# Kernel optimization log

Hardware: AMD Instinct MI355X
Metric: run time of the kernel (lower is better)

## Reference

```python
import jax, jax.numpy as jnp
import numpy as np

D_MODEL = 768
D_HEAD = 64
BATCH = 2
SEQ = 4096


def setup_inputs() -> dict:
    key = jax.random.key(0)
    k1, k2, k3, k4, k5 = jax.random.split(key, 5)
    x = jax.random.normal(k1, (BATCH, SEQ, D_MODEL), dtype=jnp.float32)
    # causal mask as the module expects: (seq_len, seq_len) float, 1 where attend allowed
    mask = jnp.tril(jnp.ones((SEQ, SEQ), dtype=jnp.float32))
    # weights initialized like the module: randn / sqrt(d_model)
    scale = 1.0 / np.sqrt(D_MODEL)
    Wq = jax.random.normal(k2, (D_HEAD, D_MODEL), dtype=jnp.float32) * scale
    Wk = jax.random.normal(k3, (D_HEAD, D_MODEL), dtype=jnp.float32) * scale
    Wv = jax.random.normal(k4, (D_HEAD, D_MODEL), dtype=jnp.float32) * scale
    Wo = jax.random.normal(k5, (D_MODEL, D_HEAD), dtype=jnp.float32) * scale
    return {"x": x, "mask": mask, "Wq": Wq, "Wk": Wk, "Wv": Wv, "Wo": Wo}


def reference(x, mask, Wq, Wk, Wv, Wo):
    # q,k,v: (B, S, d_head); Linear with weight (out,in) => x @ W.T
    q = jnp.einsum('bsm,hm->bsh', x, Wq)
    k = jnp.einsum('bsm,hm->bsh', x, Wk)
    v = jnp.einsum('bsm,hm->bsh', x, Wv)
    scores = jnp.einsum('bqd,bkd->bqk', q, k) / np.sqrt(D_HEAD)  # (B,S,S)
    seq_len = x.shape[1]
    m = mask[:seq_len, :seq_len]
    # faithful to the torch code: tril(scores) - 1e10 * (1 - mask)
    scores = jnp.tril(scores) - 1e10 * (1.0 - m)
    attn = jax.nn.softmax(scores, axis=-1)
    z = jnp.einsum('bqk,bkd->bqd', attn, v)  # (B,S,d_head)
    out = jnp.einsum('bsh,mh->bsm', z, Wo)   # (B,S,d_model)
    return out
```

## Files before the change

### kernel.cpp

```cpp
#include <hip/hip_runtime.h>
#include <stdint.h>

#define SEQ 4096
#define DM 768
#define DH 64

typedef __attribute__((ext_vector_type(8))) short short8;
typedef __attribute__((ext_vector_type(4))) short short4v;
typedef __attribute__((ext_vector_type(4))) float f32x4;
typedef __attribute__((ext_vector_type(2))) uint32_t uint2v;

#define LOG2E 1.4426950408889634f

static __device__ __forceinline__ short bf16r(float f) {
  union { float f; uint32_t u; } v; v.f = f;
  uint32_t u = v.u;
  return (short)((u + 0x7FFFu + ((u >> 16) & 1u)) >> 16);
}

static __device__ __forceinline__ float bf16f(uint16_t u) {
  union { uint32_t u; float f; } v; v.u = ((uint32_t)u) << 16;
  return v.f;
}

static __device__ __forceinline__ uint32_t cvtpk(float a, float b) {
  uint32_t r;
  asm("v_cvt_pk_bf16_f32 %0, %1, %2" : "=v"(r) : "v"(a), "v"(b));
  return r;
}

static __device__ __forceinline__ int swz(int row, int b) {
  return row * 128 + (b ^ ((row & 7) << 4));
}

static __device__ __forceinline__ void glds16(const void* g, void* l) {
  __builtin_amdgcn_global_load_lds(
      (const __attribute__((address_space(1))) uint32_t*)g,
      (__attribute__((address_space(3))) uint32_t*)l, 16, 0, 0);
}

__global__ __launch_bounds__(256) void convert_w(
    const float* __restrict__ Wq, const float* __restrict__ Wk,
    const float* __restrict__ Wv, const float* __restrict__ Wo,
    uint16_t* __restrict__ Wbp, uint16_t* __restrict__ Wob) {
  int id = blockIdx.x * 256 + threadIdx.x;
  if (id < 18432) {
    int nh = id / 9216, rem = id % 9216;
    int t = rem / 768, rem2 = rem % 768;
    int r = rem2 >> 3, g = rem2 & 7;
    int row = nh * 96 + r;
    const float* src = (row < 64) ? (Wq + (size_t)row * DM)
                     : (row < 128) ? (Wk + (size_t)(row - 64) * DM)
                                   : (Wv + (size_t)(row - 128) * DM);
    const float sc = (row < 64) ? (0.125f * LOG2E) : 1.0f;
    float4 v0 = *(const float4*)(src + t * 64 + g * 8);
    float4 v1 = *(const float4*)(src + t * 64 + g * 8 + 4);
    union { uint32_t u[4]; short8 s; } pk;
    pk.u[0] = cvtpk(v0.x * sc, v0.y * sc);
    pk.u[1] = cvtpk(v0.z * sc, v0.w * sc);
    pk.u[2] = cvtpk(v1.x * sc, v1.y * sc);
    pk.u[3] = cvtpk(v1.z * sc, v1.w * sc);
    char* dst = (char*)Wbp + (size_t)nh * 147456 + t * 12288 + swz(r, g * 16);
    *(short8*)dst = pk.s;
  } else if (id < 30720) {
    int tt = id - 18432;
    int row = tt >> 4, c4 = tt & 15;
    float4 v = *(const float4*)(Wo + (size_t)row * DH + c4 * 4);
    short4v pk = { bf16r(v.x), bf16r(v.y), bf16r(v.z), bf16r(v.w) };
    *(short4v*)(Wob + (size_t)row * DH + c4 * 4) = pk;
  }
}

__global__ __launch_bounds__(256) void qkv_proj(
    const float* __restrict__ x, const uint16_t* __restrict__ Wbp,
    uint16_t* __restrict__ qg, uint16_t* __restrict__ kg, uint16_t* __restrict__ vg) {
  __shared__ char smem[49152] __attribute__((aligned(16)));
  const int tid = threadIdx.x;
  const int lane = tid & 63, wv = tid >> 6;
  const int l15 = lane & 15, l4 = lane >> 4;
  const int row0 = blockIdx.x * 32;
  const int nh = blockIdx.y;
  const char* wsrc = (const char*)Wbp + (size_t)nh * 147456;

  const int xr = tid >> 4, xc4 = tid & 15;
  const int mh = wv & 1, ng = wv >> 1;

  const float* xp0 = x + (size_t)(row0 + xr) * DM + xc4 * 4;
  const float* xp1 = x + (size_t)(row0 + 16 + xr) * DM + xc4 * 4;

  f32x4 acc[3];
  #pragma unroll
  for (int j = 0; j < 3; ++j) acc[j] = (f32x4){0.f, 0.f, 0.f, 0.f};

  float4 xrg[2][2];
  xrg[0][0] = *(const float4*)(xp0);
  xrg[0][1] = *(const float4*)(xp1);
  #pragma unroll
  for (int i = 0; i < 3; ++i)
    glds16(wsrc + i * 1024 + wv * 3072 + lane * 16,
           smem + 12288 + wv * 3072 + i * 1024);
  __builtin_amdgcn_sched_barrier(0);
  xrg[1][0] = *(const float4*)(xp0 + 64);
  xrg[1][1] = *(const float4*)(xp1 + 64);
  #pragma unroll
  for (int i = 0; i < 3; ++i)
    glds16(wsrc + 12288 + wv * 3072 + i * 1024 + lane * 16,
           smem + 12288 + 12288 + wv * 3072 + i * 1024);
  __builtin_amdgcn_sched_barrier(0);
  {
    uint2v p0 = { cvtpk(xrg[0][0].x, xrg[0][0].y), cvtpk(xrg[0][0].z, xrg[0][0].w) };
    *(uint2v*)(smem + swz(xr, xc4 * 8)) = p0;
    uint2v p1 = { cvtpk(xrg[0][1].x, xrg[0][1].y), cvtpk(xrg[0][1].z, xrg[0][1].w) };
    *(uint2v*)(smem + swz(xr + 16, xc4 * 8)) = p1;
  }

  #pragma unroll
  for (int t = 0; t < 12; ++t) {
    asm volatile("s_waitcnt lgkmcnt(0)" ::: "memory");
    if (t < 11) {
      asm volatile("s_waitcnt vmcnt(5)" ::: "memory");
    } else {
      asm volatile("s_waitcnt vmcnt(0)" ::: "memory");
    }
    __builtin_amdgcn_s_barrier();
    if (t < 10) {
      const int k2 = (t + 2) * 64;
      xrg[t & 1][0] = *(const float4*)(xp0 + k2);
      xrg[t & 1][1] = *(const float4*)(xp1 + k2);
      #pragma unroll
      for (int i = 0; i < 3; ++i)
        glds16(wsrc + (t + 2) * 12288 + wv * 3072 + i * 1024 + lane * 16,
               smem + 12288 + ((t + 2) % 3) * 12288 + wv * 3072 + i * 1024);
      __builtin_amdgcn_sched_barrier(0);
    }
    {
      char* Xl = smem + (t % 3) * 4096;
      char* Wl = smem + 12288 + (t % 3) * 12288;
      #pragma unroll
      for (int kc = 0; kc < 2; ++kc) {
        short8 af = *(const short8*)(Xl + swz(mh * 16 + l15, kc * 64 + l4 * 16));
        #pragma unroll
        for (int j = 0; j < 3; ++j) {
          int tl = ng * 3 + j;
          short8 bfv = *(const short8*)(Wl + swz(tl * 16 + l15, kc * 64 + l4 * 16));
          acc[j] = __builtin_amdgcn_mfma_f32_16x16x32_bf16(af, bfv, acc[j], 0, 0, 0);
        }
      }
    }
    if (t < 11) {
      char* Xn = smem + ((t + 1) % 3) * 4096;
      float4 a0 = xrg[(t + 1) & 1][0], a1 = xrg[(t + 1) & 1][1];
      uint2v p0 = { cvtpk(a0.x, a0.y), cvtpk(a0.z, a0.w) };
      *(uint2v*)(Xn + swz(xr, xc4 * 8)) = p0;
      uint2v p1 = { cvtpk(a1.x, a1.y), cvtpk(a1.z, a1.w) };
      *(uint2v*)(Xn + swz(xr + 16, xc4 * 8)) = p1;
    }
  }
  #pragma unroll
  for (int j = 0; j < 3; ++j) {
    int NT = nh * 6 + ng * 3 + j;
    uint16_t* dst = (NT < 4) ? qg : (NT < 8) ? kg : vg;
    int cb = (NT & 3) * 16 + l15;
    #pragma unroll
    for (int r = 0; r < 4; ++r) {
      int row = row0 + mh * 16 + l4 * 4 + r;
      dst[(size_t)row * DH + cb] = (uint16_t)bf16r(acc[j][r]);
    }
  }
}

__global__ __launch_bounds__(256) void attn_split(
    const uint16_t* __restrict__ qg, const uint16_t* __restrict__ kg,
    const uint16_t* __restrict__ vg, uint16_t* __restrict__ zg,
    uint16_t* __restrict__ Opart, float* __restrict__ Ml, int CHUNK, int MAXCH) {
  __shared__ char smem[32768] __attribute__((aligned(16)));

  const int tid = threadIdx.x;
  const int lane = tid & 63, wv = tid >> 6;
  const int l15 = lane & 15, l4 = lane >> 4;
  const int qt = blockIdx.x, ch = blockIdx.y, b = blockIdx.z;
  const int q0 = qt << 6;
  const int kv_lim = q0 + 64;
  const int kv_begin = ch * CHUNK;
  if (kv_begin >= kv_lim) return;
  const int kv_end = min(kv_begin + CHUNK, kv_lim);
  const int ntiles = (kv_end - kv_begin) >> 6;

  const uint16_t* qb = qg + (size_t)b * SEQ * DH;
  const uint16_t* kb = kg + (size_t)b * SEQ * DH;
  const uint16_t* vb = vg + (size_t)b * SEQ * DH;

  const int qrow = q0 + wv * 16 + l15;
  short8 qf0 = *(const short8*)(qb + (size_t)qrow * DH + l4 * 8);
  short8 qf1 = *(const short8*)(qb + (size_t)qrow * DH + 32 + l4 * 8);

  int koffA[4], koffB[4], voffA[4], voffB[4];
  #pragma unroll
  for (int n = 0; n < 4; ++n) {
    koffA[n] = swz(n * 16 + l15, l4 * 16);
    koffB[n] = swz(n * 16 + l15, 64 + l4 * 16);
    int dr = n * 16 + l15;
    voffA[n] = 8192 + dr * 128 + ((l4 * 16) ^ ((dr & 7) << 4));
    voffB[n] = 8192 + dr * 128 + ((64 + l4 * 16) ^ ((dr & 7) << 4));
  }

  const int ku = tid - 128;
  const int kvgV = tid >> 4, dqV = tid & 15;
  short8 sreg[4];
  short4v vr8[8];
  int soff[4], vwoff[4];
  if (tid >= 128) {
    #pragma unroll
    for (int i = 0; i < 4; ++i) {
      int c = ku + (i << 7);
      soff[i] = swz(c >> 3, (c & 7) * 16);
    }
  } else {
    #pragma unroll
    for (int c = 0; c < 4; ++c)
      vwoff[c] = 8192 + swz(dqV * 4 + c, kvgV * 16);
  }

#define LOAD_REGS(KV0)                                                               \
  if (tid >= 128) {                                                                  \
    _Pragma("unroll")                                                                \
    for (int i = 0; i < 4; ++i) {                                                    \
      int c = ku + (i << 7);                                                         \
      sreg[i] = *(const short8*)(kb + (size_t)((KV0) + (c >> 3)) * DH + (c & 7) * 8);  \
    }                                                                                \
  } else {                                                                           \
    _Pragma("unroll")                                                                \
    for (int i = 0; i < 8; ++i)                                                      \
      vr8[i] = *(const short4v*)(vb + (size_t)((KV0) + kvgV * 8 + i) * DH + dqV * 4);  \
  }

#define STAGE_WRITE(BUF)                                                             \
  {                                                                                  \
    char* base_ = smem + ((BUF) << 14);                                              \
    if (tid >= 128) {                                                                \
      _Pragma("unroll")                                                              \
      for (int i = 0; i < 4; ++i) *(short8*)(base_ + soff[i]) = sreg[i];             \
    } else {                                                                         \
      _Pragma("unroll")                                                              \
      for (int c = 0; c < 4; ++c) {                                                  \
        short8 w;                                                                    \
        _Pragma("unroll")                                                            \
        for (int i = 0; i < 8; ++i) w[i] = vr8[i][c];                                \
        *(short8*)(base_ + vwoff[c]) = w;                                            \
      }                                                                              \
    }                                                                                \
  }

  LOAD_REGS(kv_begin);
  STAGE_WRITE(0);

  f32x4 oaccT[4];
  #pragma unroll
  for (int n = 0; n < 4; ++n) oaccT[n] = (f32x4){0.f, 0.f, 0.f, 0.f};
  float lrun = 0.f;

  const int bp0 = (((l4 & 1) << 5) + l15) << 2;
  const int bp1 = bp0 + 64;
  const bool hi2 = (l4 >> 1) != 0;

  for (int T = 0; T < ntiles; ++T) {
    const int kv0 = kv_begin + (T << 6);
    const bool more = (T + 1 < ntiles);
    if (more) { LOAD_REGS(kv0 + 64); }
    __syncthreads();
    char* cb_ = smem + ((T & 1) << 14);

    f32x4 sacc[4];
    #pragma unroll
    for (int n = 0; n < 4; ++n) sacc[n] = (f32x4){0.f, 0.f, 0.f, 0.f};
    __builtin_amdgcn_s_setprio(1);
    #pragma unroll
    for (int n = 0; n < 4; ++n) {
      short8 kf0 = *(const short8*)(cb_ + koffA[n]);
      sacc[n] = __builtin_amdgcn_mfma_f32_16x16x32_bf16(kf0, qf0, sacc[n], 0, 0, 0);
      short8 kf1 = *(const short8*)(cb_ + koffB[n]);
      sacc[n] = __builtin_amdgcn_mfma_f32_16x16x32_bf16(kf1, qf1, sacc[n], 0, 0, 0);
    }
    __builtin_amdgcn_s_setprio(0);

    if (more) { STAGE_WRITE((T + 1) & 1); }

    if (kv0 + 63 > q0) {
      #pragma unroll
      for (int n = 0; n < 4; ++n) {
        #pragma unroll
        for (int r = 0; r < 4; ++r) {
          int kvg_ = kv0 + n * 16 + l4 * 4 + r;
          if (kvg_ > qrow) sacc[n][r] = -1e30f;
        }
      }
    }

    float ls = 0.f;
    #pragma unroll
    for (int n = 0; n < 4; ++n) {
      #pragma unroll
      for (int r = 0; r < 4; ++r) {
        float p = __builtin_amdgcn_exp2f(sacc[n][r]);
        sacc[n][r] = p;
        ls += p;
      }
    }
    ls += __shfl_xor(ls, 16);
    ls += __shfl_xor(ls, 32);
    lrun += ls;

    uint32_t pk[8];
    #pragma unroll
    for (int n = 0; n < 4; ++n) {
      pk[n * 2]     = cvtpk(sacc[n][0], sacc[n][1]);
      pk[n * 2 + 1] = cvtpk(sacc[n][2], sacc[n][3]);
    }
    union { uint32_t d[4]; short8 s; } pa0u, pa1u;
    {
      uint32_t x0 = __builtin_amdgcn_ds_bpermute(bp0, (int)pk[0]);
      uint32_t x2 = __builtin_amdgcn_ds_bpermute(bp0, (int)pk[2]);
      pa0u.d[0] = hi2 ? x2 : x0;
      uint32_t y1 = __builtin_amdgcn_ds_bpermute(bp0, (int)pk[1]);
      uint32_t y3 = __builtin_amdgcn_ds_bpermute(bp0, (int)pk[3]);
      pa0u.d[1] = hi2 ? y3 : y1;
      uint32_t z0 = __builtin_amdgcn_ds_bpermute(bp1, (int)pk[0]);
      uint32_t z2 = __builtin_amdgcn_ds_bpermute(bp1, (int)pk[2]);
      pa0u.d[2] = hi2 ? z2 : z0;
      uint32_t w1 = __builtin_amdgcn_ds_bpermute(bp1, (int)pk[1]);
      uint32_t w3 = __builtin_amdgcn_ds_bpermute(bp1, (int)pk[3]);
      pa0u.d[3] = hi2 ? w3 : w1;
      uint32_t x4 = __builtin_amdgcn_ds_bpermute(bp0, (int)pk[4]);
      uint32_t x6 = __builtin_amdgcn_ds_bpermute(bp0, (int)pk[6]);
      pa1u.d[0] = hi2 ? x6 : x4;
      uint32_t y5 = __builtin_amdgcn_ds_bpermute(bp0, (int)pk[5]);
      uint32_t y7 = __builtin_amdgcn_ds_bpermute(bp0, (int)pk[7]);
      pa1u.d[1] = hi2 ? y7 : y5;
      uint32_t z4 = __builtin_amdgcn_ds_bpermute(bp1, (int)pk[4]);
      uint32_t z6 = __builtin_amdgcn_ds_bpermute(bp1, (int)pk[6]);
      pa1u.d[2] = hi2 ? z6 : z4;
      uint32_t w5 = __builtin_amdgcn_ds_bpermute(bp1, (int)pk[5]);
      uint32_t w7 = __builtin_amdgcn_ds_bpermute(bp1, (int)pk[7]);
      pa1u.d[3] = hi2 ? w7 : w5;
    }
    __builtin_amdgcn_s_setprio(1);
    #pragma unroll
    for (int n = 0; n < 4; ++n) {
      short8 vf0 = *(const short8*)(cb_ + voffA[n]);
      oaccT[n] = __builtin_amdgcn_mfma_f32_16x16x32_bf16(vf0, pa0u.s, oaccT[n], 0, 0, 0);
      short8 vf1 = *(const short8*)(cb_ + voffB[n]);
      oaccT[n] = __builtin_amdgcn_mfma_f32_16x16x32_bf16(vf1, pa1u.s, oaccT[n], 0, 0, 0);
    }
    __builtin_amdgcn_s_setprio(0);
  }
#undef LOAD_REGS
#undef STAGE_WRITE

  const int rl = wv * 16 + l15;
  if (MAXCH == 1) {
    float invl = 1.0f / lrun;
    uint16_t* zb = zg + (size_t)b * SEQ * DH;
    #pragma unroll
    for (int n = 0; n < 4; ++n) {
      short4v pkv = { bf16r(oaccT[n][0] * invl), bf16r(oaccT[n][1] * invl),
                      bf16r(oaccT[n][2] * invl), bf16r(oaccT[n][3] * invl) };
      *(short4v*)(zb + (size_t)(q0 + rl) * DH + n * 16 + l4 * 4) = pkv;
    }
  } else {
    const size_t slot = ((size_t)(b << 6) + qt) * MAXCH + ch;
    uint16_t* op = Opart + slot * 4096;
    #pragma unroll
    for (int n = 0; n < 4; ++n) {
      short4v pkv = { bf16r(oaccT[n][0]), bf16r(oaccT[n][1]),
                      bf16r(oaccT[n][2]), bf16r(oaccT[n][3]) };
      *(short4v*)(op + (size_t)rl * 64 + n * 16 + l4 * 4) = pkv;
    }
    if (l4 == 0) Ml[slot * 64 + rl] = lrun;
  }
}

__global__ __launch_bounds__(256) void out_proj(
    const uint16_t* __restrict__ Opart, const float* __restrict__ Ml,
    const uint16_t* __restrict__ zg, const uint16_t* __restrict__ Wob,
    float* __restrict__ out, int CHUNK, int MAXCH) {
  __shared__ char smem[4096 + 32768] __attribute__((aligned(16)));
  char* Zl = smem;
  char* Wl = smem + 4096;
  const int tid = threadIdx.x;
  const int lane = tid & 63, wv = tid >> 6;
  const int l15 = lane & 15, l4 = lane >> 4;
  const int row0 = blockIdx.x * 32;
  const int col0 = blockIdx.y * 256;

  {
    const int r = tid >> 3, c0 = (tid & 7) << 3;
    if (MAXCH == 1) {
      short8 v = *(const short8*)(zg + (size_t)(row0 + r) * DH + c0);
      *(short8*)(Zl + swz(r, c0 * 2)) = v;
    } else {
      const int b = row0 >> 12;
      const int rlb = row0 & 4095;
      const int qt = rlb >> 6, q0 = qt << 6;
      const int row_local = (rlb & 63) + r;
      const int nch = (q0 + 64 + CHUNK - 1) / CHUNK;
      const size_t sbase = ((size_t)(b << 6) + qt) * MAXCH;
      float a[8] = {0.f, 0.f, 0.f, 0.f, 0.f, 0.f, 0.f, 0.f};
      float wsum = 0.f;
      for (int ch = 0; ch < nch; ++ch) {
        const size_t s = sbase + ch;
        wsum += Ml[s * 64 + row_local];
        short8 v = *(const short8*)(Opart + s * 4096 + (size_t)row_local * 64 + c0);
        #pragma unroll
        for (int j = 0; j < 8; ++j) a[j] += bf16f((uint16_t)v[j]);
      }
      float inv = 1.0f / wsum;
      short8 pk;
      #pragma unroll
      for (int j = 0; j < 8; ++j) pk[j] = bf16r(a[j] * inv);
      *(short8*)(Zl + swz(r, c0 * 2)) = pk;
    }
  }
  #pragma unroll
  for (int i = 0; i < 8; ++i) {
    int id = tid + (i << 8);
    int m = id >> 3, c8 = id & 7;
    short8 vw = *(const short8*)(Wob + (size_t)(col0 + m) * DH + c8 * 8);
    *(short8*)(Wl + swz(m, c8 * 16)) = vw;
  }
  __syncthreads();

  const int mh = wv & 1, ng = wv >> 1;
  short8 af0 = *(const short8*)(Zl + swz(mh * 16 + l15, l4 * 16));
  short8 af1 = *(const short8*)(Zl + swz(mh * 16 + l15, 64 + l4 * 16));
  f32x4 acc[8];
  #pragma unroll
  for (int j = 0; j < 8; ++j) acc[j] = (f32x4){0.f, 0.f, 0.f, 0.f};
  #pragma unroll
  for (int j = 0; j < 8; ++j) {
    int nt = ng * 8 + j;
    short8 b0 = *(const short8*)(Wl + swz(nt * 16 + l15, l4 * 16));
    acc[j] = __builtin_amdgcn_mfma_f32_16x16x32_bf16(af0, b0, acc[j], 0, 0, 0);
    short8 b1 = *(const short8*)(Wl + swz(nt * 16 + l15, 64 + l4 * 16));
    acc[j] = __builtin_amdgcn_mfma_f32_16x16x32_bf16(af1, b1, acc[j], 0, 0, 0);
  }
  #pragma unroll
  for (int j = 0; j < 8; ++j) {
    int nt = ng * 8 + j;
    #pragma unroll
    for (int r = 0; r < 4; ++r) {
      int row = row0 + mh * 16 + l4 * 4 + r;
      int col = col0 + nt * 16 + l15;
      out[(size_t)row * DM + col] = acc[j][r];
    }
  }
}

extern "C" void kernel_launch(void* const* d_in, const int* in_sizes, int n_in,
                              void* d_out, int out_size, void* d_ws, size_t ws_size,
                              hipStream_t stream) {
  const float* x  = (const float*)d_in[0];
  const float* Wq = (const float*)d_in[2];
  const float* Wk = (const float*)d_in[3];
  const float* Wv = (const float*)d_in[4];
  const float* Wo = (const float*)d_in[5];
  float* out = (float*)d_out;

  const size_t N = (size_t)2 * SEQ * DH;
  uint16_t* qg = (uint16_t*)d_ws;
  uint16_t* kg = qg + N;
  uint16_t* vg = kg + N;
  uint16_t* zg = vg + N;
  uint16_t* Wbp = zg + N;
  const size_t WBE = (size_t)192 * DM;
  uint16_t* Wob = Wbp + WBE;
  const size_t WOE = (size_t)DM * DH;
  uint16_t* Opart = Wob + WOE;

  int maxch = 16;
  while (maxch > 1) {
    size_t slots = (size_t)2 * 64 * maxch;
    size_t need = 4 * N * 2 + WBE * 2 + WOE * 2 + slots * (4096 * 2 + 64 * 4);
    if (need <= ws_size) break;
    maxch >>= 1;
  }
  const int CHUNK = SEQ / maxch;
  float* Ml = (float*)(Opart + (size_t)2 * 64 * maxch * 4096);

  convert_w<<<120, 256, 0, stream>>>(Wq, Wk, Wv, Wo, Wbp, Wob);
  qkv_proj<<<dim3(256, 2), 256, 0, stream>>>(x, Wbp, qg, kg, vg);
  attn_split<<<dim3(64, maxch, 2), 256, 0, stream>>>(qg, kg, vg, zg, Opart, Ml,
                                                     CHUNK, maxch);
  out_proj<<<dim3(256, 3), 256, 0, stream>>>(Opart, Ml, zg, Wob, out, CHUNK, maxch);
}
```

Measured before the change: 48.10 us.

## Fuse weight bf16 conversion into projection kernels and drop convert_w launch

```diff
diff --git a/kernel.cpp b/kernel.cpp
--- a/kernel.cpp
+++ b/kernel.cpp
@@ -33,46 +33,9 @@
   return row * 128 + (b ^ ((row & 7) << 4));
 }
 
-static __device__ __forceinline__ void glds16(const void* g, void* l) {
-  __builtin_amdgcn_global_load_lds(
-      (const __attribute__((address_space(1))) uint32_t*)g,
-      (__attribute__((address_space(3))) uint32_t*)l, 16, 0, 0);
-}
-
-__global__ __launch_bounds__(256) void convert_w(
-    const float* __restrict__ Wq, const float* __restrict__ Wk,
-    const float* __restrict__ Wv, const float* __restrict__ Wo,
-    uint16_t* __restrict__ Wbp, uint16_t* __restrict__ Wob) {
-  int id = blockIdx.x * 256 + threadIdx.x;
-  if (id < 18432) {
-    int nh = id / 9216, rem = id % 9216;
-    int t = rem / 768, rem2 = rem % 768;
-    int r = rem2 >> 3, g = rem2 & 7;
-    int row = nh * 96 + r;
-    const float* src = (row < 64) ? (Wq + (size_t)row * DM)
-                     : (row < 128) ? (Wk + (size_t)(row - 64) * DM)
-                                   : (Wv + (size_t)(row - 128) * DM);
-    const float sc = (row < 64) ? (0.125f * LOG2E) : 1.0f;
-    float4 v0 = *(const float4*)(src + t * 64 + g * 8);
-    float4 v1 = *(const float4*)(src + t * 64 + g * 8 + 4);
-    union { uint32_t u[4]; short8 s; } pk;
-    pk.u[0] = cvtpk(v0.x * sc, v0.y * sc);
-    pk.u[1] = cvtpk(v0.z * sc, v0.w * sc);
-    pk.u[2] = cvtpk(v1.x * sc, v1.y * sc);
-    pk.u[3] = cvtpk(v1.z * sc, v1.w * sc);
-    char* dst = (char*)Wbp + (size_t)nh * 147456 + t * 12288 + swz(r, g * 16);
-    *(short8*)dst = pk.s;
-  } else if (id < 30720) {
-    int tt = id - 18432;
-    int row = tt >> 4, c4 = tt & 15;
-    float4 v = *(const float4*)(Wo + (size_t)row * DH + c4 * 4);
-    short4v pk = { bf16r(v.x), bf16r(v.y), bf16r(v.z), bf16r(v.w) };
-    *(short4v*)(Wob + (size_t)row * DH + c4 * 4) = pk;
-  }
-}
-
 __global__ __launch_bounds__(256) void qkv_proj(
-    const float* __restrict__ x, const uint16_t* __restrict__ Wbp,
+    const float* __restrict__ x, const float* __restrict__ Wq,
+    const float* __restrict__ Wk, const float* __restrict__ Wv,
     uint16_t* __restrict__ qg, uint16_t* __restrict__ kg, uint16_t* __restrict__ vg) {
   __shared__ char smem[49152] __attribute__((aligned(16)));
   const int tid = threadIdx.x;
@@ -80,91 +43,116 @@
   const int l15 = lane & 15, l4 = lane >> 4;
   const int row0 = blockIdx.x * 32;
   const int nh = blockIdx.y;
-  const char* wsrc = (const char*)Wbp + (size_t)nh * 147456;
 
   const int xr = tid >> 4, xc4 = tid & 15;
   const int mh = wv & 1, ng = wv >> 1;
+  const int wr0 = tid >> 3, wb16 = tid & 7;
 
   const float* xp0 = x + (size_t)(row0 + xr) * DM + xc4 * 4;
   const float* xp1 = x + (size_t)(row0 + 16 + xr) * DM + xc4 * 4;
 
+  const float* wp[3];
+  int wlds[3];
+  #pragma unroll
+  for (int i = 0; i < 3; ++i) {
+    int grow = nh * 96 + wr0 + i * 32;
+    wp[i] = (grow < 64) ? (Wq + (size_t)grow * DM)
+          : (grow < 128) ? (Wk + (size_t)(grow - 64) * DM)
+                         : (Wv + (size_t)(grow - 128) * DM);
+    wlds[i] = 4096 + swz(wr0 + i * 32, wb16 * 16);
+  }
+  const int xlds0 = swz(xr, xc4 * 8), xlds1 = swz(xr + 16, xc4 * 8);
+
   f32x4 acc[3];
   #pragma unroll
   for (int j = 0; j < 3; ++j) acc[j] = (f32x4){0.f, 0.f, 0.f, 0.f};
 
-  float4 xrg[2][2];
-  xrg[0][0] = *(const float4*)(xp0);
-  xrg[0][1] = *(const float4*)(xp1);
-  #pragma unroll
-  for (int i = 0; i < 3; ++i)
-    glds16(wsrc + i * 1024 + wv * 3072 + lane * 16,
-           smem + 12288 + wv * 3072 + i * 1024);
-  __builtin_amdgcn_sched_barrier(0);
-  xrg[1][0] = *(const float4*)(xp0 + 64);
-  xrg[1][1] = *(const float4*)(xp1 + 64);
-  #pragma unroll
-  for (int i = 0; i < 3; ++i)
-    glds16(wsrc + 12288 + wv * 3072 + i * 1024 + lane * 16,
-           smem + 12288 + 12288 + wv * 3072 + i * 1024);
-  __builtin_amdgcn_sched_barrier(0);
-  {
-    uint2v p0 = { cvtpk(xrg[0][0].x, xrg[0][0].y), cvtpk(xrg[0][0].z, xrg[0][0].w) };
-    *(uint2v*)(smem + swz(xr, xc4 * 8)) = p0;
-    uint2v p1 = { cvtpk(xrg[0][1].x, xrg[0][1].y), cvtpk(xrg[0][1].z, xrg[0][1].w) };
-    *(uint2v*)(smem + swz(xr + 16, xc4 * 8)) = p1;
-  }
-
-  #pragma unroll
-  for (int t = 0; t < 12; ++t) {
-    asm volatile("s_waitcnt lgkmcnt(0)" ::: "memory");
-    if (t < 11) {
-      asm volatile("s_waitcnt vmcnt(5)" ::: "memory");
-    } else {
-      asm volatile("s_waitcnt vmcnt(0)" ::: "memory");
-    }
-    __builtin_amdgcn_s_barrier();
-    if (t < 10) {
-      const int k2 = (t + 2) * 64;
-      xrg[t & 1][0] = *(const float4*)(xp0 + k2);
-      xrg[t & 1][1] = *(const float4*)(xp1 + k2);
-      #pragma unroll
-      for (int i = 0; i < 3; ++i)
-        glds16(wsrc + (t + 2) * 12288 + wv * 3072 + i * 1024 + lane * 16,
-               smem + 12288 + ((t + 2) % 3) * 12288 + wv * 3072 + i * 1024);
-      __builtin_amdgcn_sched_barrier(0);
-    }
-    {
-      char* Xl = smem + (t % 3) * 4096;
-      char* Wl = smem + 12288 + (t % 3) * 12288;
-      #pragma unroll
-      for (int kc = 0; kc < 2; ++kc) {
-        short8 af = *(const short8*)(Xl + swz(mh * 16 + l15, kc * 64 + l4 * 16));
-        #pragma unroll
-        for (int j = 0; j < 3; ++j) {
-          int tl = ng * 3 + j;
-          short8 bfv = *(const short8*)(Wl + swz(tl * 16 + l15, kc * 64 + l4 * 16));
-          acc[j] = __builtin_amdgcn_mfma_f32_16x16x32_bf16(af, bfv, acc[j], 0, 0, 0);
-        }
-      }
-    }
-    if (t < 11) {
-      char* Xn = smem + ((t + 1) % 3) * 4096;
-      float4 a0 = xrg[(t + 1) & 1][0], a1 = xrg[(t + 1) & 1][1];
-      uint2v p0 = { cvtpk(a0.x, a0.y), cvtpk(a0.z, a0.w) };
-      *(uint2v*)(Xn + swz(xr, xc4 * 8)) = p0;
-      uint2v p1 = { cvtpk(a1.x, a1.y), cvtpk(a1.z, a1.w) };
-      *(uint2v*)(Xn + swz(xr + 16, xc4 * 8)) = p1;
-    }
-  }
+  float4 xA0, xA1, xB0, xB1;
+  float4 wA[3][2], wB[3][2];
+
+#define ISSUE_A(K0)                                                              \
+  { xA0 = *(const float4*)(xp0 + (K0)); xA1 = *(const float4*)(xp1 + (K0));      \
+    _Pragma("unroll")                                                            \
+    for (int i = 0; i < 3; ++i) {                                                \
+      wA[i][0] = *(const float4*)(wp[i] + (K0) + wb16 * 8);                      \
+      wA[i][1] = *(const float4*)(wp[i] + (K0) + wb16 * 8 + 4);                  \
+    }                                                                            \
+    __builtin_amdgcn_sched_barrier(0); }
+#define ISSUE_B(K0)                                                              \
+  { xB0 = *(const float4*)(xp0 + (K0)); xB1 = *(const float4*)(xp1 + (K0));      \
+    _Pragma("unroll")                                                            \
+    for (int i = 0; i < 3; ++i) {                                                \
+      wB[i][0] = *(const float4*)(wp[i] + (K0) + wb16 * 8);                      \
+      wB[i][1] = *(const float4*)(wp[i] + (K0) + wb16 * 8 + 4);                  \
+    }                                                                            \
+    __builtin_amdgcn_sched_barrier(0); }
+#define WRITE_SET(X0, X1, WS, BUF)                                               \
+  { char* base_ = smem + (BUF) * 16384;                                          \
+    uint2v p0 = { cvtpk(X0.x, X0.y), cvtpk(X0.z, X0.w) };                        \
+    *(uint2v*)(base_ + xlds0) = p0;                                              \
+    uint2v p1 = { cvtpk(X1.x, X1.y), cvtpk(X1.z, X1.w) };                        \
+    *(uint2v*)(base_ + xlds1) = p1;                                              \
+    _Pragma("unroll")                                                            \
+    for (int i = 0; i < 3; ++i) {                                                \
+      union { uint32_t u[4]; short8 s; } pk;                                     \
+      pk.u[0] = cvtpk(WS[i][0].x, WS[i][0].y);                                   \
+      pk.u[1] = cvtpk(WS[i][0].z, WS[i][0].w);                                   \
+      pk.u[2] = cvtpk(WS[i][1].x, WS[i][1].y);                                   \
+      pk.u[3] = cvtpk(WS[i][1].z, WS[i][1].w);                                   \
+      *(short8*)(base_ + wlds[i]) = pk.s;                                        \
+    } }
+#define COMPUTE(BUF)                                                             \
+  { char* base_ = smem + (BUF) * 16384;                                          \
+    _Pragma("unroll")                                                            \
+    for (int kc = 0; kc < 2; ++kc) {                                             \
+      short8 af = *(const short8*)(base_ + swz(mh * 16 + l15, kc * 64 + l4 * 16)); \
+      _Pragma("unroll")                                                          \
+      for (int j = 0; j < 3; ++j) {                                              \
+        int tl = ng * 3 + j;                                                     \
+        short8 bfv = *(const short8*)(base_ + 4096 +                             \
+                                      swz(tl * 16 + l15, kc * 64 + l4 * 16));    \
+        acc[j] = __builtin_amdgcn_mfma_f32_16x16x32_bf16(af, bfv, acc[j], 0, 0, 0); \
+      }                                                                          \
+    } }
+#define QSTEP(T, IS, X0, X1, WS, BUFW)                                           \
+  { asm volatile("s_waitcnt lgkmcnt(0)" ::: "memory");                           \
+    __builtin_amdgcn_s_barrier();                                                \
+    if ((T) < 10) { IS(((T) + 2) * 64); }                                        \
+    COMPUTE((T) % 3);                                                            \
+    if ((T) < 11) { WRITE_SET(X0, X1, WS, (BUFW)); } }
+
+  ISSUE_A(0);
+  ISSUE_B(64);
+  WRITE_SET(xA0, xA1, wA, 0);
+
+  QSTEP(0,  ISSUE_A, xB0, xB1, wB, 1);
+  QSTEP(1,  ISSUE_B, xA0, xA1, wA, 2);
+  QSTEP(2,  ISSUE_A, xB0, xB1, wB, 0);
+  QSTEP(3,  ISSUE_B, xA0, xA1, wA, 1);
+  QSTEP(4,  ISSUE_A, xB0, xB1, wB, 2);
+  QSTEP(5,  ISSUE_B, xA0, xA1, wA, 0);
+  QSTEP(6,  ISSUE_A, xB0, xB1, wB, 1);
+  QSTEP(7,  ISSUE_B, xA0, xA1, wA, 2);
+  QSTEP(8,  ISSUE_A, xB0, xB1, wB, 0);
+  QSTEP(9,  ISSUE_B, xA0, xA1, wA, 1);
+  QSTEP(10, ISSUE_A, xB0, xB1, wB, 2);
+  QSTEP(11, ISSUE_B, xA0, xA1, wA, 0);
+#undef ISSUE_A
+#undef ISSUE_B
+#undef WRITE_SET
+#undef COMPUTE
+#undef QSTEP
+
   #pragma unroll
   for (int j = 0; j < 3; ++j) {
     int NT = nh * 6 + ng * 3 + j;
     uint16_t* dst = (NT < 4) ? qg : (NT < 8) ? kg : vg;
+    const float sc = (NT < 4) ? (0.125f * LOG2E) : 1.0f;
     int cb = (NT & 3) * 16 + l15;
     #pragma unroll
     for (int r = 0; r < 4; ++r) {
       int row = row0 + mh * 16 + l4 * 4 + r;
-      dst[(size_t)row * DH + cb] = (uint16_t)bf16r(acc[j][r]);
+      dst[(size_t)row * DH + cb] = (uint16_t)bf16r(acc[j][r] * sc);
     }
   }
 }
@@ -381,7 +369,7 @@
 
 __global__ __launch_bounds__(256) void out_proj(
     const uint16_t* __restrict__ Opart, const float* __restrict__ Ml,
-    const uint16_t* __restrict__ zg, const uint16_t* __restrict__ Wob,
+    const uint16_t* __restrict__ zg, const float* __restrict__ Wo,
     float* __restrict__ out, int CHUNK, int MAXCH) {
   __shared__ char smem[4096 + 32768] __attribute__((aligned(16)));
   char* Zl = smem;
@@ -421,11 +409,12 @@
     }
   }
   #pragma unroll
-  for (int i = 0; i < 8; ++i) {
+  for (int i = 0; i < 16; ++i) {
     int id = tid + (i << 8);
-    int m = id >> 3, c8 = id & 7;
-    short8 vw = *(const short8*)(Wob + (size_t)(col0 + m) * DH + c8 * 8);
-    *(short8*)(Wl + swz(m, c8 * 16)) = vw;
+    int m = id >> 4, c4 = id & 15;
+    float4 vw = *(const float4*)(Wo + (size_t)(col0 + m) * DH + c4 * 4);
+    uint2v pk = { cvtpk(vw.x, vw.y), cvtpk(vw.z, vw.w) };
+    *(uint2v*)(Wl + swz(m, c4 * 8)) = pk;
   }
   __syncthreads();
 
@@ -470,25 +459,20 @@
   uint16_t* kg = qg + N;
   uint16_t* vg = kg + N;
   uint16_t* zg = vg + N;
-  uint16_t* Wbp = zg + N;
-  const size_t WBE = (size_t)192 * DM;
-  uint16_t* Wob = Wbp + WBE;
-  const size_t WOE = (size_t)DM * DH;
-  uint16_t* Opart = Wob + WOE;
+  uint16_t* Opart = zg + N;
 
   int maxch = 16;
   while (maxch > 1) {
     size_t slots = (size_t)2 * 64 * maxch;
-    size_t need = 4 * N * 2 + WBE * 2 + WOE * 2 + slots * (4096 * 2 + 64 * 4);
+    size_t need = 4 * N * 2 + slots * (4096 * 2 + 64 * 4);
     if (need <= ws_size) break;
     maxch >>= 1;
   }
   const int CHUNK = SEQ / maxch;
   float* Ml = (float*)(Opart + (size_t)2 * 64 * maxch * 4096);
 
-  convert_w<<<120, 256, 0, stream>>>(Wq, Wk, Wv, Wo, Wbp, Wob);
-  qkv_proj<<<dim3(256, 2), 256, 0, stream>>>(x, Wbp, qg, kg, vg);
+  qkv_proj<<<dim3(256, 2), 256, 0, stream>>>(x, Wq, Wk, Wv, qg, kg, vg);
   attn_split<<<dim3(64, maxch, 2), 256, 0, stream>>>(qg, kg, vg, zg, Opart, Ml,
                                                      CHUNK, maxch);
-  out_proj<<<dim3(256, 3), 256, 0, stream>>>(Opart, Ml, zg, Wob, out, CHUNK, maxch);
-}
+  out_proj<<<dim3(256, 3), 256, 0, stream>>>(Opart, Ml, zg, Wo, out, CHUNK, maxch);
+}
```

Result: faster. 46.99 us (-2.3%).
